# Performance work log

Measured on AMD Instinct MI355X. Metric: run time of the kernel, lower is better.

## Reference

```python
import jax, jax.numpy as jnp
import numpy as np

ATOM_FEATURE_DIMS = [119, 5, 12, 12, 10, 6, 6, 2, 2]
N, E, H, L, PH, D, B = 200000, 640000, 128, 5, 512, 128, 8000
MAXV = max(ATOM_FEATURE_DIMS)  # 119; tables padded to common vocab for stacking
BN_EPS = 1e-5


def setup_inputs() -> dict:
    key = jax.random.key(0)
    ks = jax.random.split(key, 16)
    s = 0.05
    x = jax.random.randint(ks[0], (N, 9), 0, 2)          # valid for every slot vocab
    edge_index = jax.random.randint(ks[1], (2, E), 0, N)
    batch = jnp.sort(jax.random.randint(ks[2], (N,), 0, B))
    emb = jax.random.normal(ks[3], (9, MAXV, H), dtype=jnp.float32) * s
    eps = jnp.zeros((L,), dtype=jnp.float32)             # train_eps init 0
    w1 = jax.random.normal(ks[4], (L, H, H), dtype=jnp.float32) * s
    b1 = jnp.zeros((L, H), dtype=jnp.float32)
    w2 = jax.random.normal(ks[5], (L, H, H), dtype=jnp.float32) * s
    b2 = jnp.zeros((L, H), dtype=jnp.float32)
    gamma = jnp.ones((L, H), dtype=jnp.float32)
    beta = jnp.zeros((L, H), dtype=jnp.float32)
    pw1 = jax.random.normal(ks[6], (H, PH), dtype=jnp.float32) * s
    pb1 = jnp.zeros((PH,), dtype=jnp.float32)
    pw2 = jax.random.normal(ks[7], (PH, D), dtype=jnp.float32) * s
    pb2 = jnp.zeros((D,), dtype=jnp.float32)
    return {"x": x, "edge_index": edge_index, "batch": batch, "emb": emb,
            "eps": eps, "w1": w1, "b1": b1, "w2": w2, "b2": b2,
            "gamma": gamma, "beta": beta, "pw1": pw1, "pb1": pb1,
            "pw2": pw2, "pb2": pb2}


def _forward(x, edge_index, batch, emb, eps, w1, b1, w2, b2, gamma, beta,
             pw1, pb1, pw2, pb2):
    # AtomEncoder: sum of 9 per-slot embedding lookups -> [N, H]
    slot = jnp.arange(9)[None, :]                     # [1,9]
    h = jnp.sum(emb[slot, x], axis=1)                 # [N,9,H] -> [N,H]
    src, dst = edge_index[0], edge_index[1]
    for l in range(L):
        # GINConv: (1+eps)*x + sum_{j in N(i)} x_j, then 2-layer MLP
        agg = jax.ops.segment_sum(h[src], dst, num_segments=N)   # scatter-add
        z = (1.0 + eps[l]) * h + agg
        z = jax.nn.relu(z @ w1[l] + b1[l]) @ w2[l] + b2[l]
        # BatchNorm1d (training-mode batch statistics) + ReLU
        mu = jnp.mean(z, axis=0)
        var = jnp.var(z, axis=0)
        h = jax.nn.relu((z - mu) * jax.lax.rsqrt(var + BN_EPS) * gamma[l] + beta[l])
    # global_mean_pool over graphs
    sums = jax.ops.segment_sum(h, batch, num_segments=B)          # [B,H]
    cnt = jax.ops.segment_sum(jnp.ones((N,), h.dtype), batch, num_segments=B)
    g = sums / jnp.maximum(cnt, 1.0)[:, None]
    # projection head + L2 normalize
    g = jax.nn.relu(g @ pw1 + pb1) @ pw2 + pb2
    norm = jnp.sqrt(jnp.sum(g * g, axis=-1, keepdims=True))
    return g / jnp.maximum(norm, 1e-12)


def reference(x, edge_index, batch, emb, eps, w1, b1, w2, b2, gamma, beta,
              pw1, pb1, pw2, pb2):
    return _forward(x, edge_index, batch, emb, eps, w1, b1, w2, b2,
                    gamma, beta, pw1, pb1, pw2, pb2)
```

## Files before the change

kernel.cpp:

```cpp
#include <hip/hip_runtime.h>

#define NN 200000
#define NE 640000
#define HD 128
#define NL 5
#define PHD 512
#define NB 8000
#define MAXV 119
#define SBLK 1024
#define NBLK 782

typedef short bf16x8 __attribute__((ext_vector_type(8)));
typedef float f32x4 __attribute__((ext_vector_type(4)));

__device__ __forceinline__ void split_bf16(float f, short& hi, short& lo) {
  unsigned u = __float_as_uint(f);
  hi = (short)(u >> 16);
  float fh = __uint_as_float(u & 0xffff0000u);
  float fl = f - fh;
  unsigned ul = __float_as_uint(fl);
  lo = (short)((ul + 0x7fffu + ((ul >> 16) & 1u)) >> 16);
}

__global__ __launch_bounds__(256) void k_encoder(const int* __restrict__ x,
    const float* __restrict__ emb, float* __restrict__ h) {
  int idx = blockIdx.x * 256 + threadIdx.x;
  if (idx >= NN * HD) return;
  int n = idx >> 7, c = idx & 127;
  const int* xr = x + n * 9;
  float acc = 0.f;
#pragma unroll
  for (int s = 0; s < 9; ++s)
    acc += emb[(s * MAXV + xr[s]) * HD + c];
  h[idx] = acc;
}

__global__ __launch_bounds__(256) void k_zero_int(int* __restrict__ p, int n) {
  int i = blockIdx.x * 256 + threadIdx.x;
  if (i < n) p[i] = 0;
}

__global__ __launch_bounds__(256) void k_hist(const int* __restrict__ dst,
    int* __restrict__ deg) {
  int e = blockIdx.x * 256 + threadIdx.x;
  if (e < NE) atomicAdd(&deg[dst[e]], 1);
}

__global__ __launch_bounds__(256) void k_scan1(const int* __restrict__ deg,
    int* __restrict__ rowptr, int* __restrict__ blksum) {
  int t = threadIdx.x;
  int i = blockIdx.x * 256 + t;
  int v = (i < NN) ? deg[i] : 0;
  __shared__ int s[256];
  s[t] = v;
  __syncthreads();
  for (int off = 1; off < 256; off <<= 1) {
    int x = (t >= off) ? s[t - off] : 0;
    __syncthreads();
    s[t] += x;
    __syncthreads();
  }
  if (i < NN) rowptr[i] = s[t] - v;
  if (t == 255) blksum[blockIdx.x] = s[255];
}

__global__ __launch_bounds__(256) void k_scan2(const int* __restrict__ blksum,
    int* __restrict__ blkoff) {
  int t = threadIdx.x;
  int base = t * 4;
  int v[4];
#pragma unroll
  for (int k = 0; k < 4; ++k) v[k] = (base + k < NBLK) ? blksum[base + k] : 0;
  int p1 = v[0], p2 = p1 + v[1], p3 = p2 + v[2], tot = p3 + v[3];
  __shared__ int s[256];
  s[t] = tot;
  __syncthreads();
  for (int off = 1; off < 256; off <<= 1) {
    int x = (t >= off) ? s[t - off] : 0;
    __syncthreads();
    s[t] += x;
    __syncthreads();
  }
  int excl = s[t] - tot;
  if (base + 0 < NBLK) blkoff[base + 0] = excl;
  if (base + 1 < NBLK) blkoff[base + 1] = excl + p1;
  if (base + 2 < NBLK) blkoff[base + 2] = excl + p2;
  if (base + 3 < NBLK) blkoff[base + 3] = excl + p3;
}

__global__ __launch_bounds__(256) void k_scan3(int* __restrict__ rowptr,
    const int* __restrict__ blkoff) {
  int i = blockIdx.x * 256 + threadIdx.x;
  if (i < NN) rowptr[i] += blkoff[blockIdx.x];
  if (i == 0) rowptr[NN] = NE;
}

__global__ __launch_bounds__(256) void k_fill(const int* __restrict__ src,
    const int* __restrict__ dst, const int* __restrict__ rowptr,
    int* __restrict__ cur, int* __restrict__ csr_src) {
  int e = blockIdx.x * 256 + threadIdx.x;
  if (e >= NE) return;
  int d = dst[e];
  int pos = rowptr[d] + atomicAdd(&cur[d], 1);
  csr_src[pos] = src[e];
}

__global__ __launch_bounds__(256) void k_agg(const float* __restrict__ h,
    const int* __restrict__ rowptr, const int* __restrict__ csr_src,
    const float* __restrict__ eps, int l, float* __restrict__ A) {
  int gid = blockIdx.x * 256 + threadIdx.x;
  int node = gid >> 6, lane = gid & 63;
  if (node >= NN) return;
  float e = 1.f + eps[l];
  float2 v = ((const float2*)(h + (size_t)node * HD))[lane];
  float2 acc = make_float2(e * v.x, e * v.y);
  int beg = rowptr[node], end = rowptr[node + 1];
  for (int t = beg; t < end; ++t) {
    int j = csr_src[t];
    float2 u = ((const float2*)(h + (size_t)j * HD))[lane];
    acc.x += u.x;
    acc.y += u.y;
  }
  ((float2*)(A + (size_t)node * HD))[lane] = acc;
}

__global__ __launch_bounds__(256) void k_convw(const float* __restrict__ w1,
    const float* __restrict__ w2, short* __restrict__ wpk) {
  int idx = blockIdx.x * 256 + threadIdx.x;
  if (idx >= NL * 2 * 16384) return;
  int l = idx / (2 * 16384);
  int rem = idx % (2 * 16384);
  int mat = rem / 16384;
  int e = rem % 16384;
  int k = e >> 7, n = e & 127;
  float f = (mat ? w2 : w1)[(size_t)l * 16384 + e];
  short hi, lo;
  split_bf16(f, hi, lo);
  int kk = k >> 5, j = k & 7, kg = (k >> 3) & 3, nt = n >> 4, nc = n & 15;
  int lane = (kg << 4) | nc;
  size_t fo = (((size_t)kk * 8 + nt) * 64 + lane) * 8 + j;
  size_t base = (size_t)(l * 2 + mat) * 32768;
  wpk[base + fo] = hi;
  wpk[base + 16384 + fo] = lo;
}

template <bool RELU>
__global__ __launch_bounds__(256) void k_gemm_mfma(const float* A,
    const short* __restrict__ wpk_mat, const float* __restrict__ bias,
    float* out) {
  const int lane = threadIdx.x & 63;
  const int wid = threadIdx.x >> 6;
  const size_t row0 = (size_t)blockIdx.x * 64 + wid * 16;
  const int mrow = lane & 15;
  const int kg = lane >> 4;
  const float* Arow = A + (row0 + mrow) * HD;
  const bf16x8* wb = (const bf16x8*)wpk_mat;

  f32x4 acc[8];
#pragma unroll
  for (int i = 0; i < 8; ++i) {
    acc[i][0] = 0.f; acc[i][1] = 0.f; acc[i][2] = 0.f; acc[i][3] = 0.f;
  }

#pragma unroll
  for (int kk = 0; kk < 4; ++kk) {
    const int kbase = kk * 32 + kg * 8;
    float4 a0 = *(const float4*)(Arow + kbase);
    float4 a1 = *(const float4*)(Arow + kbase + 4);
    float av[8] = {a0.x, a0.y, a0.z, a0.w, a1.x, a1.y, a1.z, a1.w};
    bf16x8 ahi, alo;
#pragma unroll
    for (int j = 0; j < 8; ++j) {
      short hi, lo;
      split_bf16(av[j], hi, lo);
      ahi[j] = hi;
      alo[j] = lo;
    }
#pragma unroll
    for (int nt = 0; nt < 8; ++nt) {
      int f = (kk * 8 + nt) * 64 + lane;
      bf16x8 whi = wb[f];
      bf16x8 wlo = wb[2048 + f];
      acc[nt] = __builtin_amdgcn_mfma_f32_16x16x32_bf16(alo, whi, acc[nt], 0, 0, 0);
      acc[nt] = __builtin_amdgcn_mfma_f32_16x16x32_bf16(ahi, wlo, acc[nt], 0, 0, 0);
      acc[nt] = __builtin_amdgcn_mfma_f32_16x16x32_bf16(ahi, whi, acc[nt], 0, 0, 0);
    }
  }

  const int m0 = kg * 4;
  const int nc = lane & 15;
#pragma unroll
  for (int nt = 0; nt < 8; ++nt) {
    float bv = bias[nt * 16 + nc];
#pragma unroll
    for (int r = 0; r < 4; ++r) {
      float v = acc[nt][r] + bv;
      if (RELU) v = fmaxf(v, 0.f);
      out[(row0 + m0 + r) * HD + nt * 16 + nc] = v;
    }
  }
}

template <int K, int COLS, int RPT, bool RELU>
__global__ __launch_bounds__(256) void k_gemm(const float* A,
    const float* __restrict__ W, const float* __restrict__ bias,
    float* out) {
  constexpr int CG = COLS / 4;
  constexpr int RG = 256 / CG;
  constexpr int TM = RG * RPT;
  __shared__ float As[TM * K];
  const int row0 = blockIdx.x * TM;
  const float4* A4 = (const float4*)(A + (size_t)row0 * K);
  float4* As4 = (float4*)As;
  for (int i = threadIdx.x; i < TM * K / 4; i += 256) As4[i] = A4[i];
  __syncthreads();
  const int cg = threadIdx.x % CG;
  const int rg = threadIdx.x / CG;
  const int r0 = rg * RPT;
  float acc[RPT][4] = {};
  const float4* W4 = (const float4*)W;
#pragma unroll 4
  for (int k = 0; k < K; k += 4) {
    float4 w0 = W4[(size_t)(k + 0) * CG + cg];
    float4 w1 = W4[(size_t)(k + 1) * CG + cg];
    float4 w2 = W4[(size_t)(k + 2) * CG + cg];
    float4 w3 = W4[(size_t)(k + 3) * CG + cg];
#pragma unroll
    for (int r = 0; r < RPT; ++r) {
      float4 a = As4[((r0 + r) * K + k) >> 2];
      acc[r][0] += a.x * w0.x + a.y * w1.x + a.z * w2.x + a.w * w3.x;
      acc[r][1] += a.x * w0.y + a.y * w1.y + a.z * w2.y + a.w * w3.y;
      acc[r][2] += a.x * w0.z + a.y * w1.z + a.z * w2.z + a.w * w3.z;
      acc[r][3] += a.x * w0.w + a.y * w1.w + a.z * w2.w + a.w * w3.w;
    }
  }
  float4 bv = ((const float4*)bias)[cg];
#pragma unroll
  for (int r = 0; r < RPT; ++r) {
    float4 o;
    o.x = acc[r][0] + bv.x;
    o.y = acc[r][1] + bv.y;
    o.z = acc[r][2] + bv.z;
    o.w = acc[r][3] + bv.w;
    if (RELU) {
      o.x = fmaxf(o.x, 0.f); o.y = fmaxf(o.y, 0.f);
      o.z = fmaxf(o.z, 0.f); o.w = fmaxf(o.w, 0.f);
    }
    ((float4*)(out + (size_t)(row0 + r0 + r) * COLS))[cg] = o;
  }
}

__global__ __launch_bounds__(256) void k_stats1(const float* __restrict__ Z,
    float* __restrict__ partial) {
  int c = threadIdx.x & 127;
  int half = threadIdx.x >> 7;
  float s = 0.f, sq = 0.f;
  for (int n = blockIdx.x * 2 + half; n < NN; n += SBLK * 2) {
    float v = Z[(size_t)n * HD + c];
    s += v;
    sq += v * v;
  }
  __shared__ float ls[256], lq[256];
  ls[threadIdx.x] = s;
  lq[threadIdx.x] = sq;
  __syncthreads();
  if (threadIdx.x < 128) {
    partial[(size_t)blockIdx.x * 256 + threadIdx.x] =
        ls[threadIdx.x] + ls[threadIdx.x + 128];
    partial[(size_t)blockIdx.x * 256 + 128 + threadIdx.x] =
        lq[threadIdx.x] + lq[threadIdx.x + 128];
  }
}

__global__ __launch_bounds__(256) void k_stats2(const float* __restrict__ partial,
    float* __restrict__ stats) {
  int t = threadIdx.x;
  float acc = 0.f;
  for (int b = 0; b < SBLK; ++b) acc += partial[(size_t)b * 256 + t];
  stats[t] = acc;
}

__global__ __launch_bounds__(256) void k_bn(const float4* __restrict__ Z4,
    const float* __restrict__ stats, const float* __restrict__ gamma,
    const float* __restrict__ beta, float4* __restrict__ h4) {
  int idx = blockIdx.x * 256 + threadIdx.x;
  if (idx >= NN * 32) return;
  int q = idx & 31;
  float4 z = Z4[idx];
  float4 s = ((const float4*)stats)[q];
  float4 sq = ((const float4*)stats)[32 + q];
  float4 gm = ((const float4*)gamma)[q];
  float4 bt = ((const float4*)beta)[q];
  const float invn = 1.f / NN;
  float4 o;
  float mu, var;
  mu = s.x * invn; var = sq.x * invn - mu * mu;
  o.x = fmaxf((z.x - mu) * rsqrtf(var + 1e-5f) * gm.x + bt.x, 0.f);
  mu = s.y * invn; var = sq.y * invn - mu * mu;
  o.y = fmaxf((z.y - mu) * rsqrtf(var + 1e-5f) * gm.y + bt.y, 0.f);
  mu = s.z * invn; var = sq.z * invn - mu * mu;
  o.z = fmaxf((z.z - mu) * rsqrtf(var + 1e-5f) * gm.z + bt.z, 0.f);
  mu = s.w * invn; var = sq.w * invn - mu * mu;
  o.w = fmaxf((z.w - mu) * rsqrtf(var + 1e-5f) * gm.w + bt.w, 0.f);
  h4[idx] = o;
}

__global__ __launch_bounds__(256) void k_zero(float* __restrict__ p, int n) {
  int i = blockIdx.x * 256 + threadIdx.x;
  if (i < n) p[i] = 0.f;
}

__global__ __launch_bounds__(128) void k_pool(const float* __restrict__ h,
    const int* __restrict__ batch, float* __restrict__ sums) {
  int c = threadIdx.x;
  int n0 = blockIdx.x * 64;
  int nend = n0 + 64;
  if (nend > NN) nend = NN;
  int curb = batch[n0];
  float acc = 0.f;
  for (int n = n0; n < nend; ++n) {
    int b = batch[n];
    if (b != curb) {
      atomicAdd(&sums[(size_t)curb * HD + c], acc);
      acc = 0.f;
      curb = b;
    }
    acc += h[(size_t)n * HD + c];
  }
  atomicAdd(&sums[(size_t)curb * HD + c], acc);
}

__global__ __launch_bounds__(256) void k_cnt(const int* __restrict__ batch,
    float* __restrict__ cnt) {
  int n = blockIdx.x * 256 + threadIdx.x;
  if (n < NN) atomicAdd(&cnt[batch[n]], 1.f);
}

__global__ __launch_bounds__(256) void k_div(const float4* __restrict__ sums4,
    const float* __restrict__ cnt, float4* __restrict__ g4) {
  int idx = blockIdx.x * 256 + threadIdx.x;
  if (idx >= NB * 32) return;
  int b = idx >> 5;
  float inv = 1.f / fmaxf(cnt[b], 1.f);
  float4 v = sums4[idx];
  g4[idx] = make_float4(v.x * inv, v.y * inv, v.z * inv, v.w * inv);
}

__global__ __launch_bounds__(256) void k_norm(float* g) {
  int wave = threadIdx.x >> 6, lane = threadIdx.x & 63;
  int row = blockIdx.x * 4 + wave;
  if (row >= NB) return;
  float2 v = ((const float2*)(g + (size_t)row * HD))[lane];
  float sq = v.x * v.x + v.y * v.y;
#pragma unroll
  for (int o = 32; o > 0; o >>= 1) sq += __shfl_xor(sq, o, 64);
  float inv = 1.f / fmaxf(sqrtf(sq), 1e-12f);
  ((float2*)(g + (size_t)row * HD))[lane] = make_float2(v.x * inv, v.y * inv);
}

extern "C" void kernel_launch(void* const* d_in, const int* in_sizes, int n_in,
                              void* d_out, int out_size, void* d_ws, size_t ws_size,
                              hipStream_t stream) {
  const size_t need = (size_t)NN * HD * 2 + (size_t)NB * PHD + (size_t)NB * HD
                      + NB + (size_t)SBLK * 256 + 256 + (size_t)NL * 2 * 16384;
  if (ws_size < need * sizeof(float)) {
    k_zero<<<(out_size + 255) / 256, 256, 0, stream>>>((float*)d_out, out_size);
    return;
  }

  const int* x = (const int*)d_in[0];
  const int* ei = (const int*)d_in[1];
  const int* batch = (const int*)d_in[2];
  const float* emb = (const float*)d_in[3];
  const float* eps = (const float*)d_in[4];
  const float* w1 = (const float*)d_in[5];
  const float* b1 = (const float*)d_in[6];
  const float* w2 = (const float*)d_in[7];
  const float* b2 = (const float*)d_in[8];
  const float* gamma = (const float*)d_in[9];
  const float* beta = (const float*)d_in[10];
  const float* pw1 = (const float*)d_in[11];
  const float* pb1 = (const float*)d_in[12];
  const float* pw2 = (const float*)d_in[13];
  const float* pb2 = (const float*)d_in[14];
  float* out = (float*)d_out;

  float* h = (float*)d_ws;
  float* A = h + (size_t)NN * HD;
  float* g1 = A + (size_t)NN * HD;
  float* sums = g1 + (size_t)NB * PHD;
  float* cnt = sums + (size_t)NB * HD;
  float* partial = cnt + NB;
  float* stats = partial + (size_t)SBLK * 256;
  short* wpk = (short*)(stats + 256);
  float* g = out;

  int* rowptr = (int*)g1;
  int* cur = rowptr + NN + 1;
  int* blksum = cur + NN;
  int* blkoff = blksum + 1024;
  int* csr_src = blkoff + 1024;

  const int* src = ei;
  const int* dst = ei + NE;

  k_zero_int<<<(NN + 255) / 256, 256, 0, stream>>>(cur, NN);
  k_hist<<<(NE + 255) / 256, 256, 0, stream>>>(dst, cur);
  k_scan1<<<NBLK, 256, 0, stream>>>(cur, rowptr, blksum);
  k_scan2<<<1, 256, 0, stream>>>(blksum, blkoff);
  k_scan3<<<NBLK, 256, 0, stream>>>(rowptr, blkoff);
  k_zero_int<<<(NN + 255) / 256, 256, 0, stream>>>(cur, NN);
  k_fill<<<(NE + 255) / 256, 256, 0, stream>>>(src, dst, rowptr, cur, csr_src);

  k_convw<<<(NL * 2 * 16384 + 255) / 256, 256, 0, stream>>>(w1, w2, wpk);

  k_encoder<<<(NN * HD + 255) / 256, 256, 0, stream>>>(x, emb, h);

  for (int l = 0; l < NL; ++l) {
    k_agg<<<(NN * 64 + 255) / 256, 256, 0, stream>>>(h, rowptr, csr_src, eps, l, A);
    k_gemm_mfma<true><<<NN / 64, 256, 0, stream>>>(
        A, wpk + (size_t)(l * 2 + 0) * 32768, b1 + (size_t)l * HD, A);
    k_gemm_mfma<false><<<NN / 64, 256, 0, stream>>>(
        A, wpk + (size_t)(l * 2 + 1) * 32768, b2 + (size_t)l * HD, A);
    k_stats1<<<SBLK, 256, 0, stream>>>(A, partial);
    k_stats2<<<1, 256, 0, stream>>>(partial, stats);
    k_bn<<<(NN * 32 + 255) / 256, 256, 0, stream>>>(
        (const float4*)A, stats, gamma + (size_t)l * HD, beta + (size_t)l * HD,
        (float4*)h);
  }

  k_zero<<<(NB * HD + NB + 255) / 256, 256, 0, stream>>>(sums, NB * HD + NB);
  k_pool<<<NN / 64, 128, 0, stream>>>(h, batch, sums);
  k_cnt<<<(NN + 255) / 256, 256, 0, stream>>>(batch, cnt);
  k_div<<<(NB * 32 + 255) / 256, 256, 0, stream>>>(
      (const float4*)sums, cnt, (float4*)g);

  k_gemm<128, 512, 8, true><<<NB / 16, 256, 0, stream>>>(g, pw1, pb1, g1);
  k_gemm<512, 128, 2, false><<<NB / 16, 256, 0, stream>>>(g1, pw2, pb2, g);
  k_norm<<<(NB + 3) / 4, 256, 0, stream>>>(g);
}
```

Baseline: 1.747 ms.

## Fuse BN statistics into GEMM epilogue and apply BN inside aggregation

The second MFMA GEMM now computes per-block column sums and sums of squares in its epilogue, which replaces the separate stats pass over Z. A new parallel reduction kernel folds the 3125 per-block partials into the final stats. The BatchNorm+ReLU apply is folded into the next layer's neighbor aggregation and into the final pooling, with ping-pong buffers, which removes the standalone BN kernel and its full read/write of the node features. In exchange, the affine+ReLU is recomputed for every gathered neighbor, and partials are stored in the sums region, which is zeroed again before pooling.

```diff
diff --git a/kernel.cpp b/kernel.cpp
--- a/kernel.cpp
+++ b/kernel.cpp
@@ -9,6 +9,7 @@
 #define MAXV 119
 #define SBLK 1024
 #define NBLK 782
+#define GBLK (NN / 64)
 
 typedef short bf16x8 __attribute__((ext_vector_type(8)));
 typedef float f32x4 __attribute__((ext_vector_type(4)));
@@ -120,6 +121,38 @@
     float2 u = ((const float2*)(h + (size_t)j * HD))[lane];
     acc.x += u.x;
     acc.y += u.y;
+  }
+  ((float2*)(A + (size_t)node * HD))[lane] = acc;
+}
+
+__global__ __launch_bounds__(256) void k_agg_bn(const float* __restrict__ Z,
+    const int* __restrict__ rowptr, const int* __restrict__ csr_src,
+    const float* __restrict__ eps, int l, const float* __restrict__ stats,
+    const float* __restrict__ gamma, const float* __restrict__ beta,
+    float* __restrict__ A) {
+  int gid = blockIdx.x * 256 + threadIdx.x;
+  int node = gid >> 6, lane = gid & 63;
+  if (node >= NN) return;
+  const float invn = 1.f / NN;
+  int c0 = lane * 2;
+  float mu0 = stats[c0] * invn, mu1 = stats[c0 + 1] * invn;
+  float va0 = stats[128 + c0] * invn - mu0 * mu0;
+  float va1 = stats[128 + c0 + 1] * invn - mu1 * mu1;
+  float a0 = gamma[c0] * rsqrtf(va0 + 1e-5f);
+  float a1 = gamma[c0 + 1] * rsqrtf(va1 + 1e-5f);
+  float b0 = beta[c0] - mu0 * a0;
+  float b1 = beta[c0 + 1] - mu1 * a1;
+  float e = 1.f + eps[l];
+  float2 z = ((const float2*)(Z + (size_t)node * HD))[lane];
+  float2 acc;
+  acc.x = e * fmaxf(z.x * a0 + b0, 0.f);
+  acc.y = e * fmaxf(z.y * a1 + b1, 0.f);
+  int beg = rowptr[node], end = rowptr[node + 1];
+  for (int t = beg; t < end; ++t) {
+    int j = csr_src[t];
+    float2 u = ((const float2*)(Z + (size_t)j * HD))[lane];
+    acc.x += fmaxf(u.x * a0 + b0, 0.f);
+    acc.y += fmaxf(u.y * a1 + b1, 0.f);
   }
   ((float2*)(A + (size_t)node * HD))[lane] = acc;
 }
@@ -144,10 +177,10 @@
   wpk[base + 16384 + fo] = lo;
 }
 
-template <bool RELU>
+template <bool RELU, bool STATS>
 __global__ __launch_bounds__(256) void k_gemm_mfma(const float* A,
     const short* __restrict__ wpk_mat, const float* __restrict__ bias,
-    float* out) {
+    float* out, float* __restrict__ partial) {
   const int lane = threadIdx.x & 63;
   const int wid = threadIdx.x >> 6;
   const size_t row0 = (size_t)blockIdx.x * 64 + wid * 16;
@@ -189,16 +222,58 @@
 
   const int m0 = kg * 4;
   const int nc = lane & 15;
+  __shared__ float bs[4][128];
+  __shared__ float bq[4][128];
+  float sarr[8], qarr[8];
 #pragma unroll
   for (int nt = 0; nt < 8; ++nt) {
     float bv = bias[nt * 16 + nc];
+    float s = 0.f, q = 0.f;
 #pragma unroll
     for (int r = 0; r < 4; ++r) {
       float v = acc[nt][r] + bv;
       if (RELU) v = fmaxf(v, 0.f);
       out[(row0 + m0 + r) * HD + nt * 16 + nc] = v;
-    }
-  }
+      if (STATS) { s += v; q += v * v; }
+    }
+    if (STATS) { sarr[nt] = s; qarr[nt] = q; }
+  }
+  if (STATS) {
+#pragma unroll
+    for (int nt = 0; nt < 8; ++nt) {
+      float s = sarr[nt], q = qarr[nt];
+      s += __shfl_xor(s, 16); s += __shfl_xor(s, 32);
+      q += __shfl_xor(q, 16); q += __shfl_xor(q, 32);
+      if (lane < 16) {
+        bs[wid][nt * 16 + lane] = s;
+        bq[wid][nt * 16 + lane] = q;
+      }
+    }
+    __syncthreads();
+    int t = threadIdx.x;
+    if (t < 128)
+      partial[(size_t)blockIdx.x * 256 + t] =
+          bs[0][t] + bs[1][t] + bs[2][t] + bs[3][t];
+    else
+      partial[(size_t)blockIdx.x * 256 + t] =
+          bq[0][t - 128] + bq[1][t - 128] + bq[2][t - 128] + bq[3][t - 128];
+  }
+}
+
+__global__ __launch_bounds__(256) void k_stats2b(const float* __restrict__ partial,
+    float* __restrict__ stats) {
+  int col = blockIdx.x;
+  float acc = 0.f;
+  for (int b = threadIdx.x; b < GBLK; b += 256)
+    acc += partial[(size_t)b * 256 + col];
+  __shared__ float s[256];
+  s[threadIdx.x] = acc;
+  __syncthreads();
+  for (int off = 128; off > 0; off >>= 1) {
+    if (threadIdx.x < off) s[threadIdx.x] += s[threadIdx.x + off];
+    __syncthreads();
+  }
+  if (threadIdx.x == 0) stats[col] = s[0];
 }
 
 template <int K, int COLS, int RPT, bool RELU>
@@ -250,82 +325,34 @@
   }
 }
 
-__global__ __launch_bounds__(256) void k_stats1(const float* __restrict__ Z,
-    float* __restrict__ partial) {
-  int c = threadIdx.x & 127;
-  int half = threadIdx.x >> 7;
-  float s = 0.f, sq = 0.f;
-  for (int n = blockIdx.x * 2 + half; n < NN; n += SBLK * 2) {
-    float v = Z[(size_t)n * HD + c];
-    s += v;
-    sq += v * v;
-  }
-  __shared__ float ls[256], lq[256];
-  ls[threadIdx.x] = s;
-  lq[threadIdx.x] = sq;
-  __syncthreads();
-  if (threadIdx.x < 128) {
-    partial[(size_t)blockIdx.x * 256 + threadIdx.x] =
-        ls[threadIdx.x] + ls[threadIdx.x + 128];
-    partial[(size_t)blockIdx.x * 256 + 128 + threadIdx.x] =
-        lq[threadIdx.x] + lq[threadIdx.x + 128];
-  }
-}
-
-__global__ __launch_bounds__(256) void k_stats2(const float* __restrict__ partial,
-    float* __restrict__ stats) {
-  int t = threadIdx.x;
-  float acc = 0.f;
-  for (int b = 0; b < SBLK; ++b) acc += partial[(size_t)b * 256 + t];
-  stats[t] = acc;
-}
-
-__global__ __launch_bounds__(256) void k_bn(const float4* __restrict__ Z4,
-    const float* __restrict__ stats, const float* __restrict__ gamma,
-    const float* __restrict__ beta, float4* __restrict__ h4) {
-  int idx = blockIdx.x * 256 + threadIdx.x;
-  if (idx >= NN * 32) return;
-  int q = idx & 31;
-  float4 z = Z4[idx];
-  float4 s = ((const float4*)stats)[q];
-  float4 sq = ((const float4*)stats)[32 + q];
-  float4 gm = ((const float4*)gamma)[q];
-  float4 bt = ((const float4*)beta)[q];
-  const float invn = 1.f / NN;
-  float4 o;
-  float mu, var;
-  mu = s.x * invn; var = sq.x * invn - mu * mu;
-  o.x = fmaxf((z.x - mu) * rsqrtf(var + 1e-5f) * gm.x + bt.x, 0.f);
-  mu = s.y * invn; var = sq.y * invn - mu * mu;
-  o.y = fmaxf((z.y - mu) * rsqrtf(var + 1e-5f) * gm.y + bt.y, 0.f);
-  mu = s.z * invn; var = sq.z * invn - mu * mu;
-  o.z = fmaxf((z.z - mu) * rsqrtf(var + 1e-5f) * gm.z + bt.z, 0.f);
-  mu = s.w * invn; var = sq.w * invn - mu * mu;
-  o.w = fmaxf((z.w - mu) * rsqrtf(var + 1e-5f) * gm.w + bt.w, 0.f);
-  h4[idx] = o;
-}
-
 __global__ __launch_bounds__(256) void k_zero(float* __restrict__ p, int n) {
   int i = blockIdx.x * 256 + threadIdx.x;
   if (i < n) p[i] = 0.f;
 }
 
-__global__ __launch_bounds__(128) void k_pool(const float* __restrict__ h,
-    const int* __restrict__ batch, float* __restrict__ sums) {
+__global__ __launch_bounds__(128) void k_pool_bn(const float* __restrict__ Z,
+    const float* __restrict__ stats, const float* __restrict__ gamma,
+    const float* __restrict__ beta, const int* __restrict__ batch,
+    float* __restrict__ sums) {
   int c = threadIdx.x;
+  const float invn = 1.f / NN;
+  float mu = stats[c] * invn;
+  float va = stats[128 + c] * invn - mu * mu;
+  float a = gamma[c] * rsqrtf(va + 1e-5f);
+  float b = beta[c] - mu * a;
   int n0 = blockIdx.x * 64;
   int nend = n0 + 64;
   if (nend > NN) nend = NN;
   int curb = batch[n0];
   float acc = 0.f;
   for (int n = n0; n < nend; ++n) {
-    int b = batch[n];
-    if (b != curb) {
+    int bb = batch[n];
+    if (bb != curb) {
       atomicAdd(&sums[(size_t)curb * HD + c], acc);
       acc = 0.f;
-      curb = b;
-    }
-    acc += h[(size_t)n * HD + c];
+      curb = bb;
+    }
+    acc += fmaxf(Z[(size_t)n * HD + c] * a + b, 0.f);
   }
   atomicAdd(&sums[(size_t)curb * HD + c], acc);
 }
@@ -390,10 +417,12 @@
   float* g1 = A + (size_t)NN * HD;
   float* sums = g1 + (size_t)NB * PHD;
   float* cnt = sums + (size_t)NB * HD;
-  float* partial = cnt + NB;
-  float* stats = partial + (size_t)SBLK * 256;
+  float* legacy = cnt + NB;
+  float* stats = legacy + (size_t)SBLK * 256;
   short* wpk = (short*)(stats + 256);
   float* g = out;
+
+  float* partial = sums;
 
   int* rowptr = (int*)g1;
   int* cur = rowptr + NN + 1;
@@ -416,21 +445,28 @@
 
   k_encoder<<<(NN * HD + 255) / 256, 256, 0, stream>>>(x, emb, h);
 
+  float* P = h;
+  float* Q = A;
   for (int l = 0; l < NL; ++l) {
-    k_agg<<<(NN * 64 + 255) / 256, 256, 0, stream>>>(h, rowptr, csr_src, eps, l, A);
-    k_gemm_mfma<true><<<NN / 64, 256, 0, stream>>>(
-        A, wpk + (size_t)(l * 2 + 0) * 32768, b1 + (size_t)l * HD, A);
-    k_gemm_mfma<false><<<NN / 64, 256, 0, stream>>>(
-        A, wpk + (size_t)(l * 2 + 1) * 32768, b2 + (size_t)l * HD, A);
-    k_stats1<<<SBLK, 256, 0, stream>>>(A, partial);
-    k_stats2<<<1, 256, 0, stream>>>(partial, stats);
-    k_bn<<<(NN * 32 + 255) / 256, 256, 0, stream>>>(
-        (const float4*)A, stats, gamma + (size_t)l * HD, beta + (size_t)l * HD,
-        (float4*)h);
+    if (l == 0)
+      k_agg<<<(NN * 64 + 255) / 256, 256, 0, stream>>>(
+          P, rowptr, csr_src, eps, l, Q);
+    else
+      k_agg_bn<<<(NN * 64 + 255) / 256, 256, 0, stream>>>(
+          P, rowptr, csr_src, eps, l, stats,
+          gamma + (size_t)(l - 1) * HD, beta + (size_t)(l - 1) * HD, Q);
+    k_gemm_mfma<true, false><<<GBLK, 256, 0, stream>>>(
+        Q, wpk + (size_t)(l * 2 + 0) * 32768, b1 + (size_t)l * HD, Q, nullptr);
+    k_gemm_mfma<false, true><<<GBLK, 256, 0, stream>>>(
+        Q, wpk + (size_t)(l * 2 + 1) * 32768, b2 + (size_t)l * HD, Q, partial);
+    k_stats2b<<<256, 256, 0, stream>>>(partial, stats);
+    float* tmp = P; P = Q; Q = tmp;
   }
 
   k_zero<<<(NB * HD + NB + 255) / 256, 256, 0, stream>>>(sums, NB * HD + NB);
-  k_pool<<<NN / 64, 128, 0, stream>>>(h, batch, sums);
+  k_pool_bn<<<NN / 64, 128, 0, stream>>>(
+      P, stats, gamma + (size_t)(NL - 1) * HD, beta + (size_t)(NL - 1) * HD,
+      batch, sums);
   k_cnt<<<(NN + 255) / 256, 256, 0, stream>>>(batch, cnt);
   k_div<<<(NB * 32 + 255) / 256, 256, 0, stream>>>(
       (const float4*)sums, cnt, (float4*)g);
```

Result: faster. 1.415 ms (-19.0%).
